# Performance work log

Measured on AMD Instinct MI355X. Metric: run time of the kernel, lower is better.

The kernel has to match this reference:

```python
import jax, jax.numpy as jnp
import numpy as np

SIGMA = 0.4  # hp.guided_attention_sigma


def setup_inputs() -> dict:
    key = jax.random.key(0)
    k1, k2, k3 = jax.random.split(key, 3)
    B, T, S = 32, 2048, 512  # batch, trg(mel) len, src(text) len
    source_len = jax.random.randint(k1, (B,), 1, S + 1)
    target_len = jax.random.randint(k2, (B,), 1, T + 1)
    predict_attns = jax.random.uniform(k3, (B, T, S), dtype=jnp.float32)
    return {"source_len": source_len, "target_len": target_len,
            "predict_attns": predict_attns}


def reference(source_len, target_len, predict_attns):
    B, T, S = predict_attns.shape
    # grid_x indexes the output (trg) axis, grid_y the input (src) axis
    x = jnp.arange(T, dtype=jnp.float32)[None, :, None]  # [1,T,1]
    y = jnp.arange(S, dtype=jnp.float32)[None, None, :]  # [1,1,S]
    ilen = source_len.astype(jnp.float32)[:, None, None]  # [B,1,1]
    olen = target_len.astype(jnp.float32)[:, None, None]  # [B,1,1]
    # guided attention weight, zero-padded outside each sample's (olen, ilen) box
    w = 1.0 - jnp.exp(-((y / ilen - x / olen) ** 2) / (2.0 * SIGMA ** 2))
    valid = (x < olen) & (y < ilen)  # [B,T,S] non-pad mask
    w = jnp.where(valid, w, 0.0)
    # masked_select(...).mean(): sum over valid positions / count of valid positions
    num = jnp.sum(w * predict_attns)
    den = jnp.sum(valid).astype(jnp.float32)
    return num / den
```

## Files before the change

kernel.cpp:

```cpp
#include <hip/hip_runtime.h>
#include <hip/hip_bf16.h>


#define GA_T 2048
#define GA_S 512
#define GA_INV2S2 (1.0f / (2.0f * 0.4f * 0.4f))

#define BLOCK 256
#define NBLK 2048
#define GA_B 32

typedef float f32x4 __attribute__((ext_vector_type(4)));

__global__ __launch_bounds__(BLOCK) void ga_partial_kernel(
    const int* __restrict__ slen, const int* __restrict__ tlen,
    const float* __restrict__ p, float* __restrict__ partial) {
  __shared__ unsigned pref[GA_B + 1];
  __shared__ unsigned Wsh[GA_B];
  __shared__ int ilsh[GA_B];
  __shared__ float inv_il_sh[GA_B], inv_ol_sh[GA_B];

  const int tid = threadIdx.x;

  if (tid < 64) {
    unsigned sz = 0;
    if (tid < GA_B) {
      const int il = slen[tid];
      const int ol = tlen[tid];
      const unsigned W = (unsigned)((il + 3) >> 2);
      Wsh[tid] = W;
      ilsh[tid] = il;
      inv_il_sh[tid] = 1.0f / (float)il;
      inv_ol_sh[tid] = 1.0f / (float)ol;
      sz = W * (unsigned)ol;
    }
    unsigned v = sz;
#pragma unroll
    for (int d = 1; d < 32; d <<= 1) {
      unsigned u = __shfl_up(v, d, 64);
      v += (tid >= d) ? u : 0u;
    }
    if (tid < GA_B) pref[tid + 1] = v;
    if (tid == 0) pref[0] = 0;
  }
  __syncthreads();

  const unsigned S_tot = pref[GA_B];
  const unsigned chunk = (S_tot + NBLK - 1) / NBLK;
  const unsigned start = (unsigned)blockIdx.x * chunk;
  const unsigned end = (start + chunk < S_tot) ? (start + chunk) : S_tot;
  const unsigned ITERS = (chunk + BLOCK - 1) / BLOCK;

  float acc = 0.0f;

  for (unsigned it0 = 0; it0 < ITERS; it0 += 4) {
    f32x4 pv[4];
    float xo[4], invil[4], ok[4], m1[4], m2[4], m3[4];
    int s0v[4];
#pragma unroll
    for (int j = 0; j < 4; ++j) {
      const unsigned it = it0 + (unsigned)j;
      const unsigned q = start + it * BLOCK + (unsigned)tid;
      const bool valid = (it < ITERS) && (q < end);
      ok[j] = valid ? 1.0f : 0.0f;
      const unsigned qc = valid ? q : (S_tot - 1);
      int b = 0;
#pragma unroll
      for (int step = 16; step > 0; step >>= 1)
        if (pref[b + step] <= qc) b += step;
      const unsigned qr = qc - pref[b];
      const unsigned W = Wsh[b];
      const unsigned t = qr / W;
      const unsigned sv = qr - t * W;
      const int s0 = (int)(sv << 2);
      const int il = ilsh[b];
      s0v[j] = s0;
      invil[j] = inv_il_sh[b];
      xo[j] = (float)t * inv_ol_sh[b];
      m1[j] = (s0 + 1 < il) ? 1.0f : 0.0f;
      m2[j] = (s0 + 2 < il) ? 1.0f : 0.0f;
      m3[j] = (s0 + 3 < il) ? 1.0f : 0.0f;
      pv[j] = __builtin_nontemporal_load(reinterpret_cast<const f32x4*>(
          p + ((size_t)(b * GA_T + (int)t) * GA_S + s0)));
    }
#pragma unroll
    for (int j = 0; j < 4; ++j) {
      const float d0 = (float)(s0v[j] + 0) * invil[j] - xo[j];
      const float d1 = (float)(s0v[j] + 1) * invil[j] - xo[j];
      const float d2 = (float)(s0v[j] + 2) * invil[j] - xo[j];
      const float d3 = (float)(s0v[j] + 3) * invil[j] - xo[j];
      const float e0 = __expf(-(d0 * d0) * GA_INV2S2);
      const float e1 = __expf(-(d1 * d1) * GA_INV2S2);
      const float e2 = __expf(-(d2 * d2) * GA_INV2S2);
      const float e3 = __expf(-(d3 * d3) * GA_INV2S2);
      const float p0 = ok[j] * pv[j][0];
      const float p1 = ok[j] * m1[j] * pv[j][1];
      const float p2 = ok[j] * m2[j] * pv[j][2];
      const float p3 = ok[j] * m3[j] * pv[j][3];
      acc += p0 - p0 * e0;
      acc += p1 - p1 * e1;
      acc += p2 - p2 * e2;
      acc += p3 - p3 * e3;
    }
  }

  for (int off = 32; off > 0; off >>= 1)
    acc += __shfl_down(acc, off, 64);

  __shared__ float wsum[BLOCK / 64];
  const int lane = threadIdx.x & 63;
  const int wid = threadIdx.x >> 6;
  if (lane == 0) wsum[wid] = acc;
  __syncthreads();

  if (threadIdx.x == 0)
    partial[blockIdx.x] = (wsum[0] + wsum[1]) + (wsum[2] + wsum[3]);
}

__global__ __launch_bounds__(64) void ga_final_kernel(
    const int* __restrict__ slen, const int* __restrict__ tlen,
    const float* __restrict__ partial, int B, float* __restrict__ out) {
  const int lane = threadIdx.x;

  f32x4 f[NBLK / (64 * 4)];
#pragma unroll
  for (int k = 0; k < NBLK / (64 * 4); ++k)
    f[k] = *reinterpret_cast<const f32x4*>(partial + (k * 64 + lane) * 4);

  double s = 0.0;
#pragma unroll
  for (int k = 0; k < NBLK / (64 * 4); ++k)
    s += ((double)f[k][0] + (double)f[k][1]) +
         ((double)f[k][2] + (double)f[k][3]);

  double den = 0.0;
  if (lane < B) den = (double)slen[lane] * (double)tlen[lane];

#pragma unroll
  for (int off = 32; off > 0; off >>= 1) {
    s += __shfl_down(s, off, 64);
    den += __shfl_down(den, off, 64);
  }

  if (lane == 0) out[0] = (float)(s / den);
}

extern "C" void kernel_launch(void* const* d_in, const int* in_sizes, int n_in,
                              void* d_out, int out_size, void* d_ws, size_t ws_size,
                              hipStream_t stream) {
  const int* slen = (const int*)d_in[0];
  const int* tlen = (const int*)d_in[1];
  const float* p = (const float*)d_in[2];
  float* out = (float*)d_out;
  float* partial = (float*)d_ws;

  const int B = in_sizes[0];

  ga_partial_kernel<<<NBLK, BLOCK, 0, stream>>>(slen, tlen, p, partial);
  ga_final_kernel<<<1, 64, 0, stream>>>(slen, tlen, partial, B, out);
}
```

Before: 13.64 us.

## Assign four consecutive vec4 items per thread with incremental index walk

Each thread now handles four consecutive float4 work items. The work item is located once with a binary search and a float reciprocal divide with a correction step, and the following items are reached by incrementing sv/t/b instead of searching again. This removes the repeated per-item binary search and integer division, and the chunk size is rounded to a multiple of four. Loads become plain loads instead of nontemporal ones, and a strided tail loop covers any leftover items. The thread-contiguous access changes the coalescing pattern, since a wavefront's loads are now strided by 64 bytes per lane.

```diff
diff --git a/kernel.cpp b/kernel.cpp
--- a/kernel.cpp
+++ b/kernel.cpp
@@ -4,7 +4,7 @@
 
 #define GA_T 2048
 #define GA_S 512
-#define GA_INV2S2 (1.0f / (2.0f * 0.4f * 0.4f))
+#define GA_INV2S2 3.125f
 
 #define BLOCK 256
 #define NBLK 2048
@@ -17,8 +17,8 @@
     const float* __restrict__ p, float* __restrict__ partial) {
   __shared__ unsigned pref[GA_B + 1];
   __shared__ unsigned Wsh[GA_B];
-  __shared__ int ilsh[GA_B];
-  __shared__ float inv_il_sh[GA_B], inv_ol_sh[GA_B];
+  __shared__ unsigned olsh[GA_B];
+  __shared__ float filsh[GA_B], invilsh[GA_B], involsh[GA_B], invWsh[GA_B];
 
   const int tid = threadIdx.x;
 
@@ -29,9 +29,11 @@
       const int ol = tlen[tid];
       const unsigned W = (unsigned)((il + 3) >> 2);
       Wsh[tid] = W;
-      ilsh[tid] = il;
-      inv_il_sh[tid] = 1.0f / (float)il;
-      inv_ol_sh[tid] = 1.0f / (float)ol;
+      olsh[tid] = (unsigned)ol;
+      filsh[tid] = (float)il;
+      invilsh[tid] = 1.0f / (float)il;
+      involsh[tid] = 1.0f / (float)ol;
+      invWsh[tid] = 1.0f / (float)W;
       sz = W * (unsigned)ol;
     }
     unsigned v = sz;
@@ -46,62 +48,118 @@
   __syncthreads();
 
   const unsigned S_tot = pref[GA_B];
-  const unsigned chunk = (S_tot + NBLK - 1) / NBLK;
+  const unsigned chunk = ((S_tot + 4u * NBLK - 1) / (4u * NBLK)) * 4u;
   const unsigned start = (unsigned)blockIdx.x * chunk;
-  const unsigned end = (start + chunk < S_tot) ? (start + chunk) : S_tot;
-  const unsigned ITERS = (chunk + BLOCK - 1) / BLOCK;
+  const unsigned endq = (start + chunk < S_tot) ? (start + chunk) : S_tot;
 
   float acc = 0.0f;
 
-  for (unsigned it0 = 0; it0 < ITERS; it0 += 4) {
+  const unsigned q0 = start + 4u * (unsigned)tid;
+  if (q0 < endq) {
+    const unsigned nv = (endq - q0 < 4u) ? (endq - q0) : 4u;
+
+    int b = 0;
+#pragma unroll
+    for (int st = 16; st > 0; st >>= 1)
+      if (pref[b + st] <= q0) b += st;
+    const unsigned qr = q0 - pref[b];
+    unsigned W = Wsh[b];
+    unsigned t = (unsigned)((float)qr * invWsh[b]);
+    int sv = (int)qr - (int)(t * W);
+    if (sv < 0) { --t; sv += (int)W; }
+    else if (sv >= (int)W) { ++t; sv -= (int)W; }
+
+    unsigned ol = olsh[b];
+    float invil = invilsh[b], invol = involsh[b], fil = filsh[b];
+
     f32x4 pv[4];
-    float xo[4], invil[4], ok[4], m1[4], m2[4], m3[4];
-    int s0v[4];
+    float y0v[4], dsv[4], filv[4], fs0v[4];
 #pragma unroll
     for (int j = 0; j < 4; ++j) {
-      const unsigned it = it0 + (unsigned)j;
-      const unsigned q = start + it * BLOCK + (unsigned)tid;
-      const bool valid = (it < ITERS) && (q < end);
-      ok[j] = valid ? 1.0f : 0.0f;
-      const unsigned qc = valid ? q : (S_tot - 1);
-      int b = 0;
-#pragma unroll
-      for (int step = 16; step > 0; step >>= 1)
-        if (pref[b + step] <= qc) b += step;
-      const unsigned qr = qc - pref[b];
-      const unsigned W = Wsh[b];
-      const unsigned t = qr / W;
-      const unsigned sv = qr - t * W;
-      const int s0 = (int)(sv << 2);
-      const int il = ilsh[b];
-      s0v[j] = s0;
-      invil[j] = inv_il_sh[b];
-      xo[j] = (float)t * inv_ol_sh[b];
-      m1[j] = (s0 + 1 < il) ? 1.0f : 0.0f;
-      m2[j] = (s0 + 2 < il) ? 1.0f : 0.0f;
-      m3[j] = (s0 + 3 < il) ? 1.0f : 0.0f;
-      pv[j] = __builtin_nontemporal_load(reinterpret_cast<const f32x4*>(
-          p + ((size_t)(b * GA_T + (int)t) * GA_S + s0)));
-    }
+      pv[j] = (f32x4)(0.0f);
+      y0v[j] = 0.0f; dsv[j] = 0.0f; filv[j] = 0.0f; fs0v[j] = 0.0f;
+    }
+
 #pragma unroll
     for (int j = 0; j < 4; ++j) {
-      const float d0 = (float)(s0v[j] + 0) * invil[j] - xo[j];
-      const float d1 = (float)(s0v[j] + 1) * invil[j] - xo[j];
-      const float d2 = (float)(s0v[j] + 2) * invil[j] - xo[j];
-      const float d3 = (float)(s0v[j] + 3) * invil[j] - xo[j];
+      if ((unsigned)j < nv) {
+        const float fs0 = (float)(sv << 2);
+        fs0v[j] = fs0;
+        dsv[j] = invil;
+        filv[j] = fil;
+        y0v[j] = fs0 * invil - (float)t * invol;
+        pv[j] = *reinterpret_cast<const f32x4*>(
+            p + (((((unsigned)b << 11) + t) << 9) + (unsigned)(sv << 2)));
+        if (j < 3) {
+          if (++sv == (int)W) {
+            sv = 0;
+            if (++t == ol) {
+              t = 0;
+              if (++b < GA_B) {
+                W = Wsh[b]; ol = olsh[b];
+                invil = invilsh[b]; invol = involsh[b]; fil = filsh[b];
+              }
+            }
+          }
+        }
+      }
+    }
+
+#pragma unroll
+    for (int j = 0; j < 4; ++j) {
+      const float d0 = y0v[j];
+      const float d1 = y0v[j] + dsv[j];
+      const float d2 = fmaf(2.0f, dsv[j], y0v[j]);
+      const float d3 = fmaf(3.0f, dsv[j], y0v[j]);
       const float e0 = __expf(-(d0 * d0) * GA_INV2S2);
       const float e1 = __expf(-(d1 * d1) * GA_INV2S2);
       const float e2 = __expf(-(d2 * d2) * GA_INV2S2);
       const float e3 = __expf(-(d3 * d3) * GA_INV2S2);
-      const float p0 = ok[j] * pv[j][0];
-      const float p1 = ok[j] * m1[j] * pv[j][1];
-      const float p2 = ok[j] * m2[j] * pv[j][2];
-      const float p3 = ok[j] * m3[j] * pv[j][3];
+      const float p0 = (fs0v[j] < filv[j]) ? pv[j][0] : 0.0f;
+      const float p1 = (fs0v[j] + 1.0f < filv[j]) ? pv[j][1] : 0.0f;
+      const float p2 = (fs0v[j] + 2.0f < filv[j]) ? pv[j][2] : 0.0f;
+      const float p3 = (fs0v[j] + 3.0f < filv[j]) ? pv[j][3] : 0.0f;
       acc += p0 - p0 * e0;
       acc += p1 - p1 * e1;
       acc += p2 - p2 * e2;
       acc += p3 - p3 * e3;
     }
+  }
+
+  for (unsigned q = start + 4u * BLOCK + (unsigned)tid; q < endq; q += BLOCK) {
+    int b = 0;
+#pragma unroll
+    for (int st = 16; st > 0; st >>= 1)
+      if (pref[b + st] <= q) b += st;
+    const unsigned qr = q - pref[b];
+    const unsigned W = Wsh[b];
+    unsigned t = (unsigned)((float)qr * invWsh[b]);
+    int sv = (int)qr - (int)(t * W);
+    if (sv < 0) { --t; sv += (int)W; }
+    else if (sv >= (int)W) { ++t; sv -= (int)W; }
+    const int s0 = sv << 2;
+    const float fil = filsh[b];
+    const float invil = invilsh[b];
+    const float xo = (float)t * involsh[b];
+    const f32x4 pv = *reinterpret_cast<const f32x4*>(
+        p + (((((unsigned)b << 11) + t) << 9) + (unsigned)s0));
+    const float fs0 = (float)s0;
+    const float d0 = fs0 * invil - xo;
+    const float d1 = (fs0 + 1.0f) * invil - xo;
+    const float d2 = (fs0 + 2.0f) * invil - xo;
+    const float d3 = (fs0 + 3.0f) * invil - xo;
+    const float e0 = __expf(-(d0 * d0) * GA_INV2S2);
+    const float e1 = __expf(-(d1 * d1) * GA_INV2S2);
+    const float e2 = __expf(-(d2 * d2) * GA_INV2S2);
+    const float e3 = __expf(-(d3 * d3) * GA_INV2S2);
+    const float p0 = pv[0];
+    const float p1 = (fs0 + 1.0f < fil) ? pv[1] : 0.0f;
+    const float p2 = (fs0 + 2.0f < fil) ? pv[2] : 0.0f;
+    const float p3 = (fs0 + 3.0f < fil) ? pv[3] : 0.0f;
+    acc += p0 - p0 * e0;
+    acc += p1 - p1 * e1;
+    acc += p2 - p2 * e2;
+    acc += p3 - p3 * e3;
   }
 
   for (int off = 32; off > 0; off >>= 1)
```

Measured after the change: 13.57 us. No clear change (-0.5%).
